# Performance work log

Measured on AMD Instinct MI355X. Metric: run time of the kernel, lower is better.

## Reference

```python
import jax, jax.numpy as jnp
import numpy as np

N, M = 1024, 32
FN, FE = 64, 32
AGG_N, AGG_E = 128, 64
OUT_N, OUT_E = 64, 32


def _build_indices(n, m):
    nip, eip = [], []
    k = 0
    for i in range(1, n):
        j0 = max(0, i - m)
        nip += list(range(j0, i))
        eip += list(range(k, k + i - j0))
        k += i - j0
    n1 = np.array(nip, np.int32)
    eT = np.array(eip, np.int32)
    n2 = np.concatenate([np.full(min(i, m), i, np.int32) for i in range(1, n)])
    # padded previous-node window indices (0 = zero pad slot)
    prev_nodes = np.zeros(n * m, np.int32)
    k = 0
    for i in range(n):
        t = min(i, m)
        prev_nodes[(i + 1) * m - t:(i + 1) * m] = np.arange(k, k + t) + 1
        k += t
    n_e = k
    norm_node = np.full(n, 1.0 / m, np.float32)
    for i in range(1, m):
        norm_node[i] = 1.0 / i
    prev_edges = np.zeros(n_e * m, np.int32)
    k = 0
    e = 0
    for i in range(n):
        j0 = max(0, i - m)
        for j in range(j0, i):
            if j > j0:
                prev_edges[(e + 1) * m - (j - j0):(e + 1) * m] = np.arange(k, k + j - j0) + 1
            e += 1
        k += i - j0
    norm_edge = np.ones(n_e, np.float32)
    k = 0
    for i in range(1, n):
        t = min(i, m)
        for j in range(t):
            if j > 0:
                norm_edge[k] = 1.0 / j
            k += 1
    return n1, eT, n2, prev_nodes, norm_node, prev_edges, norm_edge, n_e

N1, ET, N2, PREV_N, NORM_N, PREV_E, NORM_E, NE = _build_indices(N, M)
N1 = jnp.asarray(N1); ET = jnp.asarray(ET); N2 = jnp.asarray(N2)
PREV_N = jnp.asarray(PREV_N); PREV_E = jnp.asarray(PREV_E)
NORM_N = jnp.asarray(NORM_N); NORM_E = jnp.asarray(NORM_E)


def setup_inputs() -> dict:
    key = jax.random.key(0)
    ks = jax.random.split(key, 20)
    s = 0.02
    inp = {
        'input_nodes': jax.random.normal(ks[0], (2, N, FN), jnp.float32),
        'input_edges': jax.random.normal(ks[1], (2, NE, FE), jnp.float32),
        # node-branch MLPs (exclude_last=False)
        'Wan1': jax.random.normal(ks[2], (2 * FN + FE, 2 * AGG_N)) * s,
        'ban1': jnp.zeros((2 * AGG_N,)),
        'Wan2': jax.random.normal(ks[3], (2 * AGG_N, AGG_N)) * s,
        'ban2': jnp.zeros((AGG_N,)),
        'Wln1': jax.random.normal(ks[4], (AGG_N + FN, AGG_N + FN)) * s,
        'bln1': jnp.zeros((AGG_N + FN,)),
        'Wln2': jax.random.normal(ks[5], (AGG_N + FN, OUT_N)) * s,
        'bln2': jnp.zeros((OUT_N,)),
        # edge-branch MLPs
        'Wae1': jax.random.normal(ks[6], (FN + FE, 2 * AGG_E)) * s,
        'bae1': jnp.zeros((2 * AGG_E,)),
        'Wae2': jax.random.normal(ks[7], (2 * AGG_E, AGG_E)) * s,
        'bae2': jnp.zeros((AGG_E,)),
        'Wle1': jax.random.normal(ks[8], (AGG_E + FE, AGG_E + FE)) * s,
        'ble1': jnp.zeros((AGG_E + FE,)),
        'Wle2': jax.random.normal(ks[9], (AGG_E + FE, OUT_E)) * s,
        'ble2': jnp.zeros((OUT_E,)),
    }
    return inp


def _mlp2(x, W1, b1, W2, b2):
    return jax.nn.relu(jax.nn.relu(x @ W1 + b1) @ W2 + b2)


def reference(input_nodes, input_edges, Wan1, ban1, Wan2, ban2, Wln1, bln1, Wln2, bln2,
              Wae1, bae1, Wae2, bae2, Wle1, ble1, Wle2, ble2):
    B = input_nodes.shape[0]
    # gather node-edge pairs [B, NE, FN+FE] and node-edge-node triples [B, NE, 2FN+FE]
    pairs = jnp.concatenate([input_nodes[:, N1], input_edges[:, ET]], axis=-1)
    triples = jnp.concatenate([input_nodes[:, N1], input_edges[:, ET], input_nodes[:, N2]], axis=-1)
    # node branch (exclude_last=False -> triples)
    hn = _mlp2(triples, Wan1, ban1, Wan2, ban2)                     # [B, NE, AGG_N]
    hn = jnp.concatenate([jnp.zeros((B, 1, AGG_N), hn.dtype), hn], axis=1)
    pn = hn[:, PREV_N].reshape(B, N, M, AGG_N).sum(axis=2)          # padded window sum
    pn = pn * NORM_N[None, :, None]
    nodes_in = jnp.concatenate([pn, input_nodes], axis=-1)
    out_nodes = _mlp2(nodes_in, Wln1, bln1, Wln2, bln2)             # activation_nodes = relu
    # edge branch (pairs)
    he = _mlp2(pairs, Wae1, bae1, Wae2, bae2)                       # [B, NE, AGG_E]
    he = jnp.concatenate([jnp.zeros((B, 1, AGG_E), he.dtype), he], axis=1)
    pe = he[:, PREV_E].reshape(B, NE, M, AGG_E).sum(axis=2)
    pe = pe * NORM_E[None, :, None]
    edges_in = jnp.concatenate([pe, input_edges], axis=-1)
    out_edges = _mlp2(edges_in, Wle1, ble1, Wle2, ble2)             # activation_edges = relu
    return out_nodes, out_edges
```

## Files before the change

### kernel.cpp

```cpp
#include <hip/hip_runtime.h>
#include <cstdint>

#define NN    1024
#define MM    32
#define NEDGE 32240
#define MROWS 64480
#define PX    168
#define PST   392
#define PLB   104
#define PHE   72

typedef unsigned short ushort_t;

typedef __bf16 bf16x8 __attribute__((ext_vector_type(8)));
typedef float  floatx4 __attribute__((ext_vector_type(4)));

__device__ __forceinline__ float b2f(ushort_t u) {
    union { unsigned int i; float f; } v; v.i = ((unsigned int)u) << 16; return v.f;
}
__device__ __forceinline__ ushort_t f2b(float f) {
    return __builtin_bit_cast(ushort_t, (__bf16)f);
}
__device__ __forceinline__ int edge_base(int i) {
    return (i <= MM) ? ((i * (i - 1)) >> 1) : (496 + (i - MM) * MM);
}

__global__ __launch_bounds__(256) void k_pack(
        const float* an1, const float* an2, const float* ae1, const float* ae2,
        const float* le1, const float* le2, const float* ln1, const float* ln2,
        const float* nodes,
        ushort_t* pan1, ushort_t* pan2, ushort_t* pae1, ushort_t* pae2,
        ushort_t* ple1, ushort_t* ple2, ushort_t* pln1, ushort_t* pln2,
        ushort_t* nodesb) {
    __shared__ float tile[32][33];
    const int bid = blockIdx.x;
    const int tid = threadIdx.x;
    if (bid < 152) {
        const float* s; ushort_t* d; int K, N, t;
        if (bid < 40)       { s = an1; d = pan1; K = 160; N = 256; t = bid;       }
        else if (bid < 72)  { s = an2; d = pan2; K = 256; N = 128; t = bid - 40;  }
        else if (bid < 84)  { s = ae1; d = pae1; K = 96;  N = 128; t = bid - 72;  }
        else if (bid < 92)  { s = ae2; d = pae2; K = 128; N = 64;  t = bid - 84;  }
        else if (bid < 101) { s = le1; d = ple1; K = 96;  N = 96;  t = bid - 92;  }
        else if (bid < 104) { s = le2; d = ple2; K = 96;  N = 32;  t = bid - 101; }
        else if (bid < 140) { s = ln1; d = pln1; K = 192; N = 192; t = bid - 104; }
        else                { s = ln2; d = pln2; K = 192; N = 64;  t = bid - 140; }
        int ntn = N >> 5;
        int tk = t / ntn, tn = t - tk * ntn;
        int k0 = tk * 32, n0 = tn * 32;
        int tx = tid & 31, ty = tid >> 5;
#pragma unroll
        for (int m = 0; m < 4; ++m)
            tile[ty + m * 8][tx] = s[(size_t)(k0 + ty + m * 8) * N + n0 + tx];
        __syncthreads();
#pragma unroll
        for (int m = 0; m < 4; ++m)
            d[(size_t)(n0 + ty + m * 8) * K + k0 + tx] = f2b(tile[tx][ty + m * 8]);
    } else {
        int i4 = (bid - 152) * 256 + tid;
        float4 v = ((const float4*)nodes)[i4];
        uint2 o;
        o.x = (unsigned)f2b(v.x) | ((unsigned)f2b(v.y) << 16);
        o.y = (unsigned)f2b(v.z) | ((unsigned)f2b(v.w) << 16);
        ((uint2*)nodesb)[i4] = o;
    }
}

__global__ __launch_bounds__(512, 4) void k_main(
        const ushort_t* __restrict__ nodesb, const float* __restrict__ edges,
        const ushort_t* __restrict__ pan1, const float* __restrict__ ban1,
        const ushort_t* __restrict__ pan2, const float* __restrict__ ban2,
        const ushort_t* __restrict__ pae1, const float* __restrict__ bae1,
        const ushort_t* __restrict__ pae2, const float* __restrict__ bae2,
        const ushort_t* __restrict__ ple1, const float* __restrict__ ble1,
        const ushort_t* __restrict__ ple2, const float* __restrict__ ble2,
        ushort_t* __restrict__ pn, float* __restrict__ out_edges) {
    __shared__ alignas(16) ushort_t X[2][32 * PX];
    __shared__ alignas(16) ushort_t H[2][32 * PST];
    __shared__ alignas(16) ushort_t HE[2][32 * PHE];
    const int tid = threadIdx.x;
    const int w = tid >> 6, l = tid & 63, lrow = l & 15, lq = l >> 4;
    const int i = blockIdx.x;
    const int t = min(i, MM);
    floatx4 zero = {0.f, 0.f, 0.f, 0.f};

    if (i == 0) {
        if (tid < 64)       ((unsigned*)pn)[tid] = 0u;
        else if (tid < 128) ((unsigned*)(pn + (size_t)1024 * 128))[tid - 64] = 0u;
        return;
    }
    const int j0 = i - t;
    const int eb0 = edge_base(i);

    bf16x8 B0[5], B1[5], B2[3];
#pragma unroll
    for (int kt = 0; kt < 5; ++kt) {
        B0[kt] = *(const bf16x8*)(pan1 + (size_t)(16 * w + lrow) * 160 + kt * 32 + lq * 8);
        B1[kt] = *(const bf16x8*)(pan1 + (size_t)(16 * (w + 8) + lrow) * 160 + kt * 32 + lq * 8);
    }
#pragma unroll
    for (int kt = 0; kt < 3; ++kt)
        B2[kt] = *(const bf16x8*)(pae1 + (size_t)(16 * w + lrow) * 96 + kt * 32 + lq * 8);
    const float c0 = ban1[16 * w + lrow];
    const float c1 = ban1[16 * (w + 8) + lrow];
    const float c2 = bae1[16 * w + lrow];

#pragma unroll
    for (int bb = 0; bb < 2; ++bb) {
        const int base = bb * NEDGE + eb0;
#pragma unroll
        for (int k = 0; k < 4; ++k) {
            int rr = w * 4 + k;
            unsigned* xr = (unsigned*)(X[bb] + rr * PX);
            const unsigned* nj = (const unsigned*)(nodesb + (size_t)(bb * NN + j0 + rr) * 64);
            const unsigned* ni = (const unsigned*)(nodesb + (size_t)(bb * NN + i) * 64);
            if (l < 32) { xr[l] = nj[l]; xr[48 + l] = ni[l]; }
            else if (l < 48) {
                float2 e = *(const float2*)(edges + (size_t)(base + rr) * 32 + 2 * (l - 32));
                xr[l] = (unsigned)f2b(e.x) | ((unsigned)f2b(e.y) << 16);
            }
        }
    }
    __syncthreads();

#pragma unroll
    for (int bb = 0; bb < 2; ++bb)
#pragma unroll
        for (int s = 0; s < 2; ++s) {
            bf16x8 A[5];
#pragma unroll
            for (int kt = 0; kt < 5; ++kt)
                A[kt] = *(const bf16x8*)&X[bb][(s * 16 + lrow) * PX + kt * 32 + lq * 8];
            floatx4 a0 = zero, a1 = zero, a2 = zero;
#pragma unroll
            for (int kt = 0; kt < 5; ++kt) {
                a0 = __builtin_amdgcn_mfma_f32_16x16x32_bf16(A[kt], B0[kt], a0, 0, 0, 0);
                a1 = __builtin_amdgcn_mfma_f32_16x16x32_bf16(A[kt], B1[kt], a1, 0, 0, 0);
            }
#pragma unroll
            for (int kt = 0; kt < 3; ++kt)
                a2 = __builtin_amdgcn_mfma_f32_16x16x32_bf16(A[kt], B2[kt], a2, 0, 0, 0);
#pragma unroll
            for (int r_ = 0; r_ < 4; ++r_) {
                int row = (s * 16 + lq * 4 + r_) * PST;
                H[bb][row + 16 * w + lrow]       = f2b(fmaxf(a0[r_] + c0, 0.f));
                H[bb][row + 128 + 16 * w + lrow] = f2b(fmaxf(a1[r_] + c1, 0.f));
                H[bb][row + 256 + 16 * w + lrow] = f2b(fmaxf(a2[r_] + c2, 0.f));
            }
        }

    bf16x8 D0[8], D1[8], E[4];
    float d0 = 0.f, d1 = 0.f, d2 = 0.f;
    if (w < 4) {
#pragma unroll
        for (int kt = 0; kt < 8; ++kt) {
            D0[kt] = *(const bf16x8*)(pan2 + (size_t)(16 * w + lrow) * 256 + kt * 32 + lq * 8);
            D1[kt] = *(const bf16x8*)(pan2 + (size_t)(16 * (w + 4) + lrow) * 256 + kt * 32 + lq * 8);
        }
        d0 = ban2[16 * w + lrow];
        d1 = ban2[16 * (w + 4) + lrow];
    } else {
        int u = w - 4;
#pragma unroll
        for (int kt = 0; kt < 4; ++kt)
            E[kt] = *(const bf16x8*)(pae2 + (size_t)(16 * u + lrow) * 128 + kt * 32 + lq * 8);
        d2 = bae2[16 * u + lrow];
    }
    __syncthreads();

    if (w < 4) {
#pragma unroll
        for (int bb = 0; bb < 2; ++bb) {
            float P0 = 0.f, P1 = 0.f;
#pragma unroll
            for (int s = 0; s < 2; ++s) {
                floatx4 a0 = zero, a1 = zero;
#pragma unroll
                for (int kt = 0; kt < 8; ++kt) {
                    bf16x8 a = *(const bf16x8*)&H[bb][(s * 16 + lrow) * PST + kt * 32 + lq * 8];
                    a0 = __builtin_amdgcn_mfma_f32_16x16x32_bf16(a, D0[kt], a0, 0, 0, 0);
                    a1 = __builtin_amdgcn_mfma_f32_16x16x32_bf16(a, D1[kt], a1, 0, 0, 0);
                }
#pragma unroll
                for (int r_ = 0; r_ < 4; ++r_) {
                    int row = s * 16 + lq * 4 + r_;
                    float v0 = b2f(f2b(fmaxf(a0[r_] + d0, 0.f)));
                    float v1 = b2f(f2b(fmaxf(a1[r_] + d1, 0.f)));
                    if (row < t) { P0 += v0; P1 += v1; }
                }
            }
            P0 += __shfl_xor(P0, 16); P0 += __shfl_xor(P0, 32);
            P1 += __shfl_xor(P1, 16); P1 += __shfl_xor(P1, 32);
            if (l < 16) {
                float inv = 1.0f / (float)t;
                pn[(size_t)(bb * 1024 + i) * 128 + 16 * w + lrow]       = f2b(P0 * inv);
                pn[(size_t)(bb * 1024 + i) * 128 + 16 * (w + 4) + lrow] = f2b(P1 * inv);
            }
        }
    } else {
        int u = w - 4;
#pragma unroll
        for (int bb = 0; bb < 2; ++bb)
#pragma unroll
            for (int s = 0; s < 2; ++s) {
                floatx4 a2 = zero;
#pragma unroll
                for (int kt = 0; kt < 4; ++kt) {
                    bf16x8 a = *(const bf16x8*)&H[bb][(s * 16 + lrow) * PST + 256 + kt * 32 + lq * 8];
                    a2 = __builtin_amdgcn_mfma_f32_16x16x32_bf16(a, E[kt], a2, 0, 0, 0);
                }
#pragma unroll
                for (int r_ = 0; r_ < 4; ++r_)
                    HE[bb][(s * 16 + lq * 4 + r_) * PHE + 16 * u + lrow] = f2b(fmaxf(a2[r_] + d2, 0.f));
            }
        if (l < 16) {
#pragma unroll
            for (int bb = 0; bb < 2; ++bb) {
                float h[32];
#pragma unroll
                for (int p = 0; p < 32; ++p)
                    h[p] = b2f(HE[bb][p * PHE + 16 * u + l]);
                float run = 0.f;
#pragma unroll
                for (int p = 0; p < 32; ++p) {
                    if (p < t)
                        X[bb][p * PX + 16 * u + l] = f2b((p == 0) ? 0.f : run * (1.0f / (float)p));
                    run += h[p];
                }
            }
        }
    }
    bf16x8 F0[3]; float v0 = 0.f;
    if (w < 6) {
#pragma unroll
        for (int kt = 0; kt < 3; ++kt)
            F0[kt] = *(const bf16x8*)(ple1 + (size_t)(16 * w + lrow) * 96 + kt * 32 + lq * 8);
        v0 = ble1[16 * w + lrow];
    }
    __syncthreads();

    if (w < 6) {
#pragma unroll
        for (int bb = 0; bb < 2; ++bb)
#pragma unroll
            for (int s = 0; s < 2; ++s) {
                bf16x8 A[3];
#pragma unroll
                for (int kt = 0; kt < 3; ++kt)
                    A[kt] = *(const bf16x8*)&X[bb][(s * 16 + lrow) * PX + kt * 32 + lq * 8];
                floatx4 a0 = zero;
#pragma unroll
                for (int kt = 0; kt < 3; ++kt)
                    a0 = __builtin_amdgcn_mfma_f32_16x16x32_bf16(A[kt], F0[kt], a0, 0, 0, 0);
#pragma unroll
                for (int r_ = 0; r_ < 4; ++r_)
                    H[bb][(s * 16 + lq * 4 + r_) * PLB + 16 * w + lrow] = f2b(fmaxf(a0[r_] + v0, 0.f));
            }
    }
    const int ct = w & 1, s2 = w >> 1, c0o = 16 * ct;
    bf16x8 F2[3]; float v2 = 0.f;
    if (w < 4) {
#pragma unroll
        for (int kt = 0; kt < 3; ++kt)
            F2[kt] = *(const bf16x8*)(ple2 + (size_t)(c0o + lrow) * 96 + kt * 32 + lq * 8);
        v2 = ble2[c0o + lrow];
    }
    __syncthreads();

    if (w < 4) {
#pragma unroll
        for (int bb = 0; bb < 2; ++bb) {
            floatx4 a2 = zero;
#pragma unroll
            for (int kt = 0; kt < 3; ++kt) {
                bf16x8 a = *(const bf16x8*)&H[bb][(s2 * 16 + lrow) * PLB + kt * 32 + lq * 8];
                a2 = __builtin_amdgcn_mfma_f32_16x16x32_bf16(a, F2[kt], a2, 0, 0, 0);
            }
            const int base = bb * NEDGE + eb0;
#pragma unroll
            for (int r_ = 0; r_ < 4; ++r_) {
                int grow = s2 * 16 + lq * 4 + r_;
                if (grow < t)
                    out_edges[(size_t)(base + grow) * 32 + c0o + lrow] = fmaxf(a2[r_] + v2, 0.f);
            }
        }
    }
}

__global__ __launch_bounds__(192) void k_final(
        const ushort_t* __restrict__ pn, const ushort_t* __restrict__ nodesb,
        const ushort_t* __restrict__ pln1, const float* __restrict__ bln1,
        const ushort_t* __restrict__ pln2, const float* __restrict__ bln2,
        float* __restrict__ out_nodes) {
    __shared__ alignas(16) ushort_t LA[32 * 200];
    __shared__ alignas(16) ushort_t LB[32 * 200];
    const int tid = threadIdx.x;
    const int w = tid >> 6, l = tid & 63, lrow = l & 15, lq = l >> 4;
    floatx4 zero = {0.f, 0.f, 0.f, 0.f};

    int tile = blockIdx.x;
    for (int u = tid; u < 768; u += 192) {
        int row = u / 24, c = u - row * 24;
        int r = tile * 32 + row;
        const uint4* src = (c < 16) ? ((const uint4*)(pn + (size_t)r * 128) + c)
                                    : ((const uint4*)(nodesb + (size_t)r * 64) + (c - 16));
        *(uint4*)&LA[row * 200 + c * 8] = *src;
    }
    bf16x8 f1[6][4]; float v1[4];
#pragma unroll
    for (int kt = 0; kt < 6; ++kt)
#pragma unroll
        for (int nt = 0; nt < 4; ++nt)
            f1[kt][nt] = *(const bf16x8*)(pln1 + (size_t)(w * 64 + nt * 16 + lrow) * 192 + kt * 32 + lq * 8);
#pragma unroll
    for (int nt = 0; nt < 4; ++nt) v1[nt] = bln1[w * 64 + nt * 16 + lrow];
    __syncthreads();

    floatx4 acc[2][4];
#pragma unroll
    for (int s = 0; s < 2; ++s)
#pragma unroll
        for (int nt = 0; nt < 4; ++nt) acc[s][nt] = zero;
#pragma unroll
    for (int s = 0; s < 2; ++s)
#pragma unroll
        for (int kt = 0; kt < 6; ++kt) {
            bf16x8 a = *(const bf16x8*)&LA[(s * 16 + lrow) * 200 + kt * 32 + lq * 8];
#pragma unroll
            for (int nt = 0; nt < 4; ++nt)
                acc[s][nt] = __builtin_amdgcn_mfma_f32_16x16x32_bf16(a, f1[kt][nt], acc[s][nt], 0, 0, 0);
        }
#pragma unroll
    for (int s = 0; s < 2; ++s)
#pragma unroll
        for (int nt = 0; nt < 4; ++nt) {
            int col = w * 64 + nt * 16 + lrow;
#pragma unroll
            for (int r_ = 0; r_ < 4; ++r_)
                LB[(s * 16 + lq * 4 + r_) * 200 + col] = f2b(fmaxf(acc[s][nt][r_] + v1[nt], 0.f));
        }
    bf16x8 f2[6][2]; float v2[2] = {0.f, 0.f};
    if (w < 2) {
#pragma unroll
        for (int kt = 0; kt < 6; ++kt)
#pragma unroll
            for (int nt = 0; nt < 2; ++nt)
                f2[kt][nt] = *(const bf16x8*)(pln2 + (size_t)(w * 32 + nt * 16 + lrow) * 192 + kt * 32 + lq * 8);
#pragma unroll
        for (int nt = 0; nt < 2; ++nt) v2[nt] = bln2[w * 32 + nt * 16 + lrow];
    }
    __syncthreads();
    if (w < 2) {
        floatx4 a2[2][2];
#pragma unroll
        for (int s = 0; s < 2; ++s) { a2[s][0] = zero; a2[s][1] = zero; }
#pragma unroll
        for (int s = 0; s < 2; ++s)
#pragma unroll
            for (int kt = 0; kt < 6; ++kt) {
                bf16x8 a = *(const bf16x8*)&LB[(s * 16 + lrow) * 200 + kt * 32 + lq * 8];
#pragma unroll
                for (int nt = 0; nt < 2; ++nt)
                    a2[s][nt] = __builtin_amdgcn_mfma_f32_16x16x32_bf16(a, f2[kt][nt], a2[s][nt], 0, 0, 0);
            }
#pragma unroll
        for (int s = 0; s < 2; ++s)
#pragma unroll
            for (int nt = 0; nt < 2; ++nt) {
                int col = w * 32 + nt * 16 + lrow;
#pragma unroll
                for (int r_ = 0; r_ < 4; ++r_)
                    out_nodes[(size_t)(tile * 32 + s * 16 + lq * 4 + r_) * 64 + col] =
                        fmaxf(a2[s][nt][r_] + v2[nt], 0.f);
            }
    }
}

extern "C" void kernel_launch(void* const* d_in, const int* in_sizes, int n_in,
                              void* d_out, int out_size, void* d_ws, size_t ws_size,
                              hipStream_t stream) {
    const float* nodes = (const float*)d_in[0];
    const float* edges = (const float*)d_in[1];
    const float* Wan1 = (const float*)d_in[2];  const float* ban1 = (const float*)d_in[3];
    const float* Wan2 = (const float*)d_in[4];  const float* ban2 = (const float*)d_in[5];
    const float* Wln1 = (const float*)d_in[6];  const float* bln1 = (const float*)d_in[7];
    const float* Wln2 = (const float*)d_in[8];  const float* bln2 = (const float*)d_in[9];
    const float* Wae1 = (const float*)d_in[10]; const float* bae1 = (const float*)d_in[11];
    const float* Wae2 = (const float*)d_in[12]; const float* bae2 = (const float*)d_in[13];
    const float* Wle1 = (const float*)d_in[14]; const float* ble1 = (const float*)d_in[15];
    const float* Wle2 = (const float*)d_in[16]; const float* ble2 = (const float*)d_in[17];

    char* ws = (char*)d_ws;
    size_t o = 0;
    auto alloc = [&](size_t bytes) -> void* {
        void* r = ws + o;
        o += (bytes + 255) & ~(size_t)255;
        return r;
    };
    ushort_t* pn     = (ushort_t*)alloc((size_t)2048 * 128 * 2);
    ushort_t* nodesb = (ushort_t*)alloc((size_t)2 * NN * 64 * 2);
    ushort_t* pan1 = (ushort_t*)alloc(160 * 256 * 2);
    ushort_t* pan2 = (ushort_t*)alloc(256 * 128 * 2);
    ushort_t* pae1 = (ushort_t*)alloc(96 * 128 * 2);
    ushort_t* pae2 = (ushort_t*)alloc(128 * 64 * 2);
    ushort_t* ple1 = (ushort_t*)alloc(96 * 96 * 2);
    ushort_t* ple2 = (ushort_t*)alloc(96 * 32 * 2);
    ushort_t* pln1 = (ushort_t*)alloc(192 * 192 * 2);
    ushort_t* pln2 = (ushort_t*)alloc(192 * 64 * 2);

    float* out_nodes = (float*)d_out;
    float* out_edges = (float*)d_out + 2 * NN * 64;

    k_pack<<<280, 256, 0, stream>>>(Wan1, Wan2, Wae1, Wae2, Wle1, Wle2, Wln1, Wln2,
                                    nodes,
                                    pan1, pan2, pae1, pae2, ple1, ple2, pln1, pln2,
                                    nodesb);
    k_main<<<1024, 512, 0, stream>>>(nodesb, edges,
                                     pan1, ban1, pan2, ban2,
                                     pae1, bae1, pae2, bae2,
                                     ple1, ble1, ple2, ble2,
                                     pn, out_edges);
    k_final<<<64, 192, 0, stream>>>(pn, nodesb, pln1, bln1, pln2, bln2, out_nodes);

    (void)in_sizes; (void)n_in; (void)out_size; (void)ws_size;
}
```

Measured before the change: 141.4 us.

## Fuse node output MLP into main kernel and drop final kernel launch

The node-branch output MLP (Wln1/Wln2) now runs inside k_main: each block writes its aggregated node features and input node row into shared memory. Idle waves 6-7 then compute the two small layers with MFMA, using a padded 16-row tile of which only two rows are real. This removes the separate k_final launch and the pn workspace round-trip through global memory. The cost is that every block reloads the Wln1/Wln2 weights from global or L2 and wastes MFMA work on padding rows. Block 0 no longer exits early, and the HE pitch shrinks to 66.

```diff
diff --git a/kernel.cpp b/kernel.cpp
--- a/kernel.cpp
+++ b/kernel.cpp
@@ -8,7 +8,7 @@
 #define PX    168
 #define PST   392
 #define PLB   104
-#define PHE   72
+#define PHE   66
 
 typedef unsigned short ushort_t;
 
@@ -74,21 +74,20 @@
         const ushort_t* __restrict__ pae2, const float* __restrict__ bae2,
         const ushort_t* __restrict__ ple1, const float* __restrict__ ble1,
         const ushort_t* __restrict__ ple2, const float* __restrict__ ble2,
-        ushort_t* __restrict__ pn, float* __restrict__ out_edges) {
+        const ushort_t* __restrict__ pln1, const float* __restrict__ bln1,
+        const ushort_t* __restrict__ pln2, const float* __restrict__ bln2,
+        float* __restrict__ out_nodes, float* __restrict__ out_edges) {
     __shared__ alignas(16) ushort_t X[2][32 * PX];
     __shared__ alignas(16) ushort_t H[2][32 * PST];
     __shared__ alignas(16) ushort_t HE[2][32 * PHE];
+    __shared__ alignas(16) ushort_t NF[2][200];
+    __shared__ alignas(16) ushort_t NF2[2][200];
     const int tid = threadIdx.x;
     const int w = tid >> 6, l = tid & 63, lrow = l & 15, lq = l >> 4;
     const int i = blockIdx.x;
     const int t = min(i, MM);
     floatx4 zero = {0.f, 0.f, 0.f, 0.f};
 
-    if (i == 0) {
-        if (tid < 64)       ((unsigned*)pn)[tid] = 0u;
-        else if (tid < 128) ((unsigned*)(pn + (size_t)1024 * 128))[tid - 64] = 0u;
-        return;
-    }
     const int j0 = i - t;
     const int eb0 = edge_base(i);
 
@@ -192,9 +191,9 @@
             P0 += __shfl_xor(P0, 16); P0 += __shfl_xor(P0, 32);
             P1 += __shfl_xor(P1, 16); P1 += __shfl_xor(P1, 32);
             if (l < 16) {
-                float inv = 1.0f / (float)t;
-                pn[(size_t)(bb * 1024 + i) * 128 + 16 * w + lrow]       = f2b(P0 * inv);
-                pn[(size_t)(bb * 1024 + i) * 128 + 16 * (w + 4) + lrow] = f2b(P1 * inv);
+                float inv = 1.0f / (float)max(t, 1);
+                NF[bb][16 * w + lrow]       = f2b(P0 * inv);
+                NF[bb][16 * (w + 4) + lrow] = f2b(P1 * inv);
             }
         }
     } else {
@@ -229,6 +228,10 @@
                 }
             }
         }
+        if (w == 7) {
+            NF[0][128 + l] = X[0][96 + l];
+            NF[1][128 + l] = X[1][96 + l];
+        }
     }
     bf16x8 F0[3]; float v0 = 0.f;
     if (w < 6) {
@@ -256,6 +259,27 @@
                 for (int r_ = 0; r_ < 4; ++r_)
                     H[bb][(s * 16 + lq * 4 + r_) * PLB + 16 * w + lrow] = f2b(fmaxf(a0[r_] + v0, 0.f));
             }
+    } else {
+        int half = w - 6;
+        bf16x8 An[6];
+#pragma unroll
+        for (int kt = 0; kt < 6; ++kt)
+            An[kt] = *(const bf16x8*)&NF[lrow & 1][kt * 32 + lq * 8];
+#pragma unroll
+        for (int nn = 0; nn < 6; ++nn) {
+            int n = half * 6 + nn;
+            floatx4 acc = zero;
+#pragma unroll
+            for (int kt = 0; kt < 6; ++kt) {
+                bf16x8 bfr = *(const bf16x8*)(pln1 + (size_t)(n * 16 + lrow) * 192 + kt * 32 + lq * 8);
+                acc = __builtin_amdgcn_mfma_f32_16x16x32_bf16(An[kt], bfr, acc, 0, 0, 0);
+            }
+            float bias = bln1[n * 16 + lrow];
+            if (lq == 0) {
+                NF2[0][n * 16 + lrow] = f2b(fmaxf(acc[0] + bias, 0.f));
+                NF2[1][n * 16 + lrow] = f2b(fmaxf(acc[1] + bias, 0.f));
+            }
+        }
     }
     const int ct = w & 1, s2 = w >> 1, c0o = 16 * ct;
     bf16x8 F2[3]; float v2 = 0.f;
@@ -284,95 +308,27 @@
                     out_edges[(size_t)(base + grow) * 32 + c0o + lrow] = fmaxf(a2[r_] + v2, 0.f);
             }
         }
-    }
-}
-
-__global__ __launch_bounds__(192) void k_final(
-        const ushort_t* __restrict__ pn, const ushort_t* __restrict__ nodesb,
-        const ushort_t* __restrict__ pln1, const float* __restrict__ bln1,
-        const ushort_t* __restrict__ pln2, const float* __restrict__ bln2,
-        float* __restrict__ out_nodes) {
-    __shared__ alignas(16) ushort_t LA[32 * 200];
-    __shared__ alignas(16) ushort_t LB[32 * 200];
-    const int tid = threadIdx.x;
-    const int w = tid >> 6, l = tid & 63, lrow = l & 15, lq = l >> 4;
-    floatx4 zero = {0.f, 0.f, 0.f, 0.f};
-
-    int tile = blockIdx.x;
-    for (int u = tid; u < 768; u += 192) {
-        int row = u / 24, c = u - row * 24;
-        int r = tile * 32 + row;
-        const uint4* src = (c < 16) ? ((const uint4*)(pn + (size_t)r * 128) + c)
-                                    : ((const uint4*)(nodesb + (size_t)r * 64) + (c - 16));
-        *(uint4*)&LA[row * 200 + c * 8] = *src;
-    }
-    bf16x8 f1[6][4]; float v1[4];
-#pragma unroll
-    for (int kt = 0; kt < 6; ++kt)
-#pragma unroll
-        for (int nt = 0; nt < 4; ++nt)
-            f1[kt][nt] = *(const bf16x8*)(pln1 + (size_t)(w * 64 + nt * 16 + lrow) * 192 + kt * 32 + lq * 8);
-#pragma unroll
-    for (int nt = 0; nt < 4; ++nt) v1[nt] = bln1[w * 64 + nt * 16 + lrow];
-    __syncthreads();
-
-    floatx4 acc[2][4];
-#pragma unroll
-    for (int s = 0; s < 2; ++s)
-#pragma unroll
-        for (int nt = 0; nt < 4; ++nt) acc[s][nt] = zero;
-#pragma unroll
-    for (int s = 0; s < 2; ++s)
-#pragma unroll
-        for (int kt = 0; kt < 6; ++kt) {
-            bf16x8 a = *(const bf16x8*)&LA[(s * 16 + lrow) * 200 + kt * 32 + lq * 8];
-#pragma unroll
-            for (int nt = 0; nt < 4; ++nt)
-                acc[s][nt] = __builtin_amdgcn_mfma_f32_16x16x32_bf16(a, f1[kt][nt], acc[s][nt], 0, 0, 0);
-        }
-#pragma unroll
-    for (int s = 0; s < 2; ++s)
-#pragma unroll
-        for (int nt = 0; nt < 4; ++nt) {
-            int col = w * 64 + nt * 16 + lrow;
-#pragma unroll
-            for (int r_ = 0; r_ < 4; ++r_)
-                LB[(s * 16 + lq * 4 + r_) * 200 + col] = f2b(fmaxf(acc[s][nt][r_] + v1[nt], 0.f));
-        }
-    bf16x8 f2[6][2]; float v2[2] = {0.f, 0.f};
-    if (w < 2) {
+    } else if (w >= 6) {
+        int half = w - 6;
+        bf16x8 A2[6];
 #pragma unroll
         for (int kt = 0; kt < 6; ++kt)
-#pragma unroll
-            for (int nt = 0; nt < 2; ++nt)
-                f2[kt][nt] = *(const bf16x8*)(pln2 + (size_t)(w * 32 + nt * 16 + lrow) * 192 + kt * 32 + lq * 8);
-#pragma unroll
-        for (int nt = 0; nt < 2; ++nt) v2[nt] = bln2[w * 32 + nt * 16 + lrow];
-    }
-    __syncthreads();
-    if (w < 2) {
-        floatx4 a2[2][2];
-#pragma unroll
-        for (int s = 0; s < 2; ++s) { a2[s][0] = zero; a2[s][1] = zero; }
-#pragma unroll
-        for (int s = 0; s < 2; ++s)
+            A2[kt] = *(const bf16x8*)&NF2[lrow & 1][kt * 32 + lq * 8];
+#pragma unroll
+        for (int nn = 0; nn < 2; ++nn) {
+            int n = half * 2 + nn;
+            floatx4 acc = zero;
 #pragma unroll
             for (int kt = 0; kt < 6; ++kt) {
-                bf16x8 a = *(const bf16x8*)&LB[(s * 16 + lrow) * 200 + kt * 32 + lq * 8];
-#pragma unroll
-                for (int nt = 0; nt < 2; ++nt)
-                    a2[s][nt] = __builtin_amdgcn_mfma_f32_16x16x32_bf16(a, f2[kt][nt], a2[s][nt], 0, 0, 0);
-            }
-#pragma unroll
-        for (int s = 0; s < 2; ++s)
-#pragma unroll
-            for (int nt = 0; nt < 2; ++nt) {
-                int col = w * 32 + nt * 16 + lrow;
-#pragma unroll
-                for (int r_ = 0; r_ < 4; ++r_)
-                    out_nodes[(size_t)(tile * 32 + s * 16 + lq * 4 + r_) * 64 + col] =
-                        fmaxf(a2[s][nt][r_] + v2[nt], 0.f);
-            }
+                bf16x8 bfr = *(const bf16x8*)(pln2 + (size_t)(n * 16 + lrow) * 192 + kt * 32 + lq * 8);
+                acc = __builtin_amdgcn_mfma_f32_16x16x32_bf16(A2[kt], bfr, acc, 0, 0, 0);
+            }
+            float bias = bln2[n * 16 + lrow];
+            if (lq == 0) {
+                out_nodes[(size_t)i * 64 + n * 16 + lrow]          = fmaxf(acc[0] + bias, 0.f);
+                out_nodes[(size_t)(1024 + i) * 64 + n * 16 + lrow] = fmaxf(acc[1] + bias, 0.f);
+            }
+        }
     }
 }
 
@@ -397,7 +353,6 @@
         o += (bytes + 255) & ~(size_t)255;
         return r;
     };
-    ushort_t* pn     = (ushort_t*)alloc((size_t)2048 * 128 * 2);
     ushort_t* nodesb = (ushort_t*)alloc((size_t)2 * NN * 64 * 2);
     ushort_t* pan1 = (ushort_t*)alloc(160 * 256 * 2);
     ushort_t* pan2 = (ushort_t*)alloc(256 * 128 * 2);
@@ -419,8 +374,8 @@
                                      pan1, ban1, pan2, ban2,
                                      pae1, bae1, pae2, bae2,
                                      ple1, ble1, ple2, ble2,
-                                     pn, out_edges);
-    k_final<<<64, 192, 0, stream>>>(pn, nodesb, pln1, bln1, pln2, bln2, out_nodes);
+                                     pln1, bln1, pln2, bln2,
+                                     out_nodes, out_edges);
 
     (void)in_sizes; (void)n_in; (void)out_size; (void)ws_size;
 }
```

New measurement: 142.4 us. About the same (+0.7%).
